# Optimization experiments

Hardware: AMD Instinct MI355X
Metric: run time of the kernel (lower is better)

The kernel has to match this reference:

```python
import jax, jax.numpy as jnp
import numpy as np
import math

B, N, D_IN, D_V, H, D_FF = 8, 2048, 256, 256, 8, 512
HD = D_V // H  # head dim = 32
EPS = 1e-5


def layernorm(x, g, b):
    mu = jnp.mean(x, axis=-1, keepdims=True)
    var = jnp.mean(jnp.square(x - mu), axis=-1, keepdims=True)
    return (x - mu) * jax.lax.rsqrt(var + EPS) * g + b


def setup_inputs() -> dict:
    key = jax.random.key(0)
    ks = jax.random.split(key, 12)
    s = 1.0 / math.sqrt(D_IN)
    return {
        "x": jax.random.normal(ks[0], (B, N, D_IN), jnp.float32),
        "y": jax.random.normal(ks[1], (B, N, D_IN), jnp.float32),
        "Wq": jax.random.normal(ks[2], (D_IN, D_V), jnp.float32) * s,
        "bq": jnp.zeros((D_V,), jnp.float32),
        "Wk": jax.random.normal(ks[3], (D_IN, D_V), jnp.float32) * s,
        "bk": jnp.zeros((D_V,), jnp.float32),
        "Wv": jax.random.normal(ks[4], (D_IN, D_V), jnp.float32) * s,
        "bv": jnp.zeros((D_V,), jnp.float32),
        "W1": jax.random.normal(ks[5], (D_V, D_FF), jnp.float32) * s,
        "b1": jnp.zeros((D_FF,), jnp.float32),
        "W2": jax.random.normal(ks[6], (D_FF, D_V), jnp.float32) * (1.0 / math.sqrt(D_FF)),
        "b2": jnp.zeros((D_V,), jnp.float32),
        "ln0_g": jnp.ones((D_IN,), jnp.float32),
        "ln0_b": jnp.zeros((D_IN,), jnp.float32),
        "ln1_g": jnp.ones((D_V,), jnp.float32),
        "ln1_b": jnp.zeros((D_V,), jnp.float32),
    }


def reference(x, y, Wq, bq, Wk, bk, Wv, bv, W1, b1, W2, b2, ln0_g, ln0_b, ln1_g, ln1_b):
    xn = layernorm(x, ln0_g, ln0_b)                      # ln0 on queries
    Q = (xn @ Wq + bq).reshape(B, N, H, HD)              # [B,Nq,H,hd]
    K = (y @ Wk + bk).reshape(B, N, H, HD)
    V = (y @ Wv + bv).reshape(B, N, H, HD)
    # NOTE: faithful scale = 1/sqrt(dim_V) (full model dim), not head dim
    S = jnp.einsum("bqhd,bkhd->bhqk", Q, K) / math.sqrt(D_V)
    A = jax.nn.softmax(S, axis=-1)
    O = Q + jnp.einsum("bhqk,bkhd->bqhd", A, V)          # per-head residual Q_ + A
    O = O.reshape(B, N, D_V)
    On = layernorm(O, ln1_g, ln1_b)
    ff = jax.nn.gelu(On @ W1 + b1, approximate=False) @ W2 + b2
    return O + ff
```

## Files before the change

kernel.cpp:

```cpp
#include <hip/hip_runtime.h>
#include <math.h>

#define RTOT 16384
#define NSEQ 2048
#define NHEAD 8
#define HDIM 32
#define QSCALE 0.09017132252479462f
#define QINV (1.0f / QSCALE)

typedef __attribute__((ext_vector_type(8))) short short8;
typedef __attribute__((ext_vector_type(4))) float f32x4;
typedef __attribute__((ext_vector_type(4))) unsigned uint4v;

#define GLOBAL_AS(p) ((__attribute__((address_space(1))) void*)(p))
#define LDS_AS(p) ((__attribute__((address_space(3))) void*)(p))

__device__ __forceinline__ unsigned pack_bf16(float a, float b) {
  unsigned ua = __float_as_uint(a) + 0x8000u;
  unsigned ub = __float_as_uint(b) + 0x8000u;
  return (ua >> 16) | (ub & 0xffff0000u);
}
__device__ __forceinline__ unsigned pack_bf16_perm(float a, float b) {
  return __builtin_amdgcn_perm(__float_as_uint(b), __float_as_uint(a),
                               0x07060302u);
}
__device__ __forceinline__ ushort bf16_1(float a) {
  return (ushort)((__float_as_uint(a) + 0x8000u) >> 16);
}
__device__ __forceinline__ float bf16_to_f(ushort u) {
  return __uint_as_float(((unsigned)u) << 16);
}
__device__ __forceinline__ short8 frag4(unsigned a0, unsigned a1, unsigned a2,
                                        unsigned a3) {
  uint4v t = {a0, a1, a2, a3};
  return __builtin_bit_cast(short8, t);
}

__global__ __launch_bounds__(256) void stage0_kernel(
    const float* __restrict__ x, const float* __restrict__ y,
    const float* __restrict__ Wq, const float* __restrict__ Wk,
    const float* __restrict__ Wv, const float* __restrict__ W1,
    const float* __restrict__ W2, const float* __restrict__ ln0g,
    const float* __restrict__ ln0b, ushort* __restrict__ Wqt,
    ushort* __restrict__ Wkt, ushort* __restrict__ Wvt,
    ushort* __restrict__ W1t, ushort* __restrict__ W2t,
    ushort* __restrict__ yh, ushort* __restrict__ xh) {
  const int bid = blockIdx.x;
  const int t = threadIdx.x;
  if (bid < 112) {
    const float* W;
    ushort* Wt;
    int K, N, tile;
    if (bid < 16) { W = Wq; Wt = Wqt; K = 256; N = 256; tile = bid; }
    else if (bid < 32) { W = Wk; Wt = Wkt; K = 256; N = 256; tile = bid - 16; }
    else if (bid < 48) { W = Wv; Wt = Wvt; K = 256; N = 256; tile = bid - 32; }
    else if (bid < 80) { W = W1; Wt = W1t; K = 256; N = 512; tile = bid - 48; }
    else { W = W2; Wt = W2t; K = 512; N = 256; tile = bid - 80; }
    const int tn = N >> 6;
    const int k0 = (tile / tn) << 6, n0 = (tile % tn) << 6;
    __shared__ float T[64][65];
#pragma unroll
    for (int i = 0; i < 16; ++i) {
      const int idx = t + i * 256;
      const int r = idx >> 6, c = idx & 63;
      T[r][c] = W[(size_t)(k0 + r) * N + n0 + c];
    }
    __syncthreads();
#pragma unroll
    for (int i = 0; i < 16; ++i) {
      const int idx = t + i * 256;
      const int r = idx >> 6, c = idx & 63;
      Wt[(size_t)(n0 + r) * K + k0 + c] = bf16_1(T[c][r]);
    }
  } else if (bid < 4208) {
    const size_t i = ((size_t)(bid - 112) * 256 + t) * 4;
    const float4 v = *(const float4*)&y[i];
    uint2 pk;
    pk.x = pack_bf16(v.x, v.y);
    pk.y = pack_bf16(v.z, v.w);
    *(uint2*)&yh[i] = pk;
  } else {
    const int lane = t & 63, wave = t >> 6;
    const size_t row = (size_t)(bid - 4208) * 4 + wave;
    const float* xr = x + row * 256;
    float4 v = *(const float4*)&xr[lane * 4];
    float s = v.x + v.y + v.z + v.w;
#pragma unroll
    for (int m = 1; m < 64; m <<= 1) s += __shfl_xor(s, m, 64);
    const float mu = s * (1.0f / 256.0f);
    const float dx = v.x - mu, dy = v.y - mu, dz = v.z - mu, dw = v.w - mu;
    float ss = dx * dx + dy * dy + dz * dz + dw * dw;
#pragma unroll
    for (int m = 1; m < 64; m <<= 1) ss += __shfl_xor(ss, m, 64);
    const float rstd = rsqrtf(ss * (1.0f / 256.0f) + 1e-5f);
    const float4 gv = *(const float4*)&ln0g[lane * 4];
    const float4 bv = *(const float4*)&ln0b[lane * 4];
    uint2 pk;
    pk.x = pack_bf16(dx * rstd * gv.x + bv.x, dy * rstd * gv.y + bv.y);
    pk.y = pack_bf16(dz * rstd * gv.z + bv.z, dw * rstd * gv.w + bv.w);
    *(uint2*)&xh[row * 256 + lane * 4] = pk;
  }
}

__global__ __launch_bounds__(256) void ln_kernel(
    const float* __restrict__ X, const float* __restrict__ g,
    const float* __restrict__ bt, ushort* __restrict__ Yh) {
  const int lane = threadIdx.x & 63;
  const int wave = threadIdx.x >> 6;
  const size_t row = (size_t)blockIdx.x * 4 + wave;
  const float* xr = X + row * 256;
  float4 v = *(const float4*)&xr[lane * 4];
  float s = v.x + v.y + v.z + v.w;
#pragma unroll
  for (int m = 1; m < 64; m <<= 1) s += __shfl_xor(s, m, 64);
  const float mu = s * (1.0f / 256.0f);
  const float dx = v.x - mu, dy = v.y - mu, dz = v.z - mu, dw = v.w - mu;
  float ss = dx * dx + dy * dy + dz * dz + dw * dw;
#pragma unroll
  for (int m = 1; m < 64; m <<= 1) ss += __shfl_xor(ss, m, 64);
  const float rstd = rsqrtf(ss * (1.0f / 256.0f) + 1e-5f);
  const float4 gv = *(const float4*)&g[lane * 4];
  const float4 bv = *(const float4*)&bt[lane * 4];
  uint2 pk;
  pk.x = pack_bf16(dx * rstd * gv.x + bv.x, dy * rstd * gv.y + bv.y);
  pk.y = pack_bf16(dz * rstd * gv.z + bv.z, dw * rstd * gv.w + bv.w);
  *(uint2*)&Yh[row * 256 + lane * 4] = pk;
}

__global__ __launch_bounds__(256) void qkv_kernel(
    const ushort* __restrict__ xh, const ushort* __restrict__ yh,
    const ushort* __restrict__ Wqt, const ushort* __restrict__ Wkt,
    const ushort* __restrict__ Wvt, const float* __restrict__ bq,
    const float* __restrict__ bk, const float* __restrict__ bv,
    ushort* __restrict__ Qh, ushort* __restrict__ Kh,
    ushort* __restrict__ VhT) {
  __shared__ union UU {
    struct { ushort As[128 * 32]; ushort Bs[64 * 32]; } s;
    ushort Ct[64 * 136];
  } u;
  const int t = threadIdx.x;
  const int lane = t & 63, wave = t >> 6;
  const int l16 = lane & 15, quad = lane >> 4;
  const int row0 = blockIdx.x * 128;
  const int ny = blockIdx.y;
  const int which = ny >> 2;
  const int n0 = (ny & 3) << 6;
  const ushort* A = (which == 2) ? xh : yh;
  const ushort* W = (which == 0) ? Wkt : (which == 1) ? Wvt : Wqt;
  const float* bs = (which == 0) ? bk : (which == 1) ? bv : bq;
  const int mrow = (wave & 1) * 64, ncol = (wave >> 1) * 32;

  const ushort* gA0 = A + (size_t)(row0 + (t >> 2)) * 256 + ((t & 3) << 3);
  const ushort* gA1 = gA0 + (size_t)64 * 256;
  const ushort* gB = W + (size_t)(n0 + (t >> 2)) * 256 + ((t & 3) << 3);
  ushort* lA0 = u.s.As + 8 * t;
  ushort* lA1 = u.s.As + 2048 + 8 * t;
  ushort* lB = u.s.Bs + 8 * t;

  f32x4 acc[4][2] = {};
  for (int kc = 0; kc < 256; kc += 32) {
    __builtin_amdgcn_global_load_lds(GLOBAL_AS(gA0 + kc), LDS_AS(lA0), 16, 0, 0);
    __builtin_amdgcn_global_load_lds(GLOBAL_AS(gA1 + kc), LDS_AS(lA1), 16, 0, 0);
    __builtin_amdgcn_global_load_lds(GLOBAL_AS(gB + kc), LDS_AS(lB), 16, 0, 0);
    __syncthreads();
    short8 af[4], bfr[2];
#pragma unroll
    for (int mi = 0; mi < 4; ++mi)
      af[mi] = *(const short8*)&u.s.As[(mrow + mi * 16 + l16) * 32 + quad * 8];
#pragma unroll
    for (int nj = 0; nj < 2; ++nj)
      bfr[nj] = *(const short8*)&u.s.Bs[(ncol + nj * 16 + l16) * 32 + quad * 8];
#pragma unroll
    for (int mi = 0; mi < 4; ++mi)
#pragma unroll
      for (int nj = 0; nj < 2; ++nj)
        acc[mi][nj] = __builtin_amdgcn_mfma_f32_16x16x32_bf16(
            af[mi], bfr[nj], acc[mi][nj], 0, 0, 0);
    __syncthreads();
  }

  if (which == 1) {
#pragma unroll
    for (int nj = 0; nj < 2; ++nj) {
      const int nloc = ncol + nj * 16 + l16;
      const float bvv = bs[n0 + nloc];
#pragma unroll
      for (int mi = 0; mi < 4; ++mi)
#pragma unroll
        for (int r = 0; r < 4; ++r)
          u.Ct[nloc * 136 + mrow + mi * 16 + quad * 4 + r] =
              bf16_1(acc[mi][nj][r] + bvv);
    }
    __syncthreads();
    const int bb = row0 >> 11, ns0 = row0 & 2047;
#pragma unroll
    for (int i = 0; i < 4; ++i) {
      const int c = t + i * 256;
      const int rr = c >> 4, c8 = (c & 15) << 3;
      *(float4*)&VhT[(size_t)(bb * 256 + n0 + rr) * 2048 + ns0 + c8] =
          *(const float4*)&u.Ct[rr * 136 + c8];
    }
  } else {
#pragma unroll
    for (int nj = 0; nj < 2; ++nj) {
      const int n = n0 + ncol + nj * 16 + l16;
      const float bvv = bs[n];
#pragma unroll
      for (int mi = 0; mi < 4; ++mi) {
#pragma unroll
        for (int r = 0; r < 4; ++r) {
          const size_t m = (size_t)row0 + mrow + mi * 16 + quad * 4 + r;
          const float v = acc[mi][nj][r] + bvv;
          if (which == 2) Qh[m * 256 + n] = bf16_1(v * QSCALE);
          else Kh[m * 256 + n] = bf16_1(v);
        }
      }
    }
  }
}

template <int MODE>
__global__ __launch_bounds__(256) void mgemm_kernel(
    const ushort* __restrict__ A, const ushort* __restrict__ Wt,
    const float* __restrict__ bias, const float* __restrict__ res,
    float* __restrict__ Cf, ushort* __restrict__ Ch, int K, int N) {
  __shared__ ushort As[128 * 32];
  __shared__ ushort Bs[64 * 32];
  const int t = threadIdx.x;
  const int lane = t & 63, wave = t >> 6;
  const int l16 = lane & 15, quad = lane >> 4;
  const int row0 = blockIdx.x * 128;
  const int n0 = blockIdx.y << 6;
  const int mrow = (wave & 1) * 64, ncol = (wave >> 1) * 32;

  const ushort* gA0 = A + (size_t)(row0 + (t >> 2)) * K + ((t & 3) << 3);
  const ushort* gA1 = gA0 + (size_t)64 * K;
  const ushort* gB = Wt + (size_t)(n0 + (t >> 2)) * K + ((t & 3) << 3);
  ushort* lA0 = As + 8 * t;
  ushort* lA1 = As + 2048 + 8 * t;
  ushort* lB = Bs + 8 * t;

  f32x4 acc[4][2] = {};
  for (int kc = 0; kc < K; kc += 32) {
    __builtin_amdgcn_global_load_lds(GLOBAL_AS(gA0 + kc), LDS_AS(lA0), 16, 0, 0);
    __builtin_amdgcn_global_load_lds(GLOBAL_AS(gA1 + kc), LDS_AS(lA1), 16, 0, 0);
    __builtin_amdgcn_global_load_lds(GLOBAL_AS(gB + kc), LDS_AS(lB), 16, 0, 0);
    __syncthreads();
    short8 af[4], bfr[2];
#pragma unroll
    for (int mi = 0; mi < 4; ++mi)
      af[mi] = *(const short8*)&As[(mrow + mi * 16 + l16) * 32 + quad * 8];
#pragma unroll
    for (int nj = 0; nj < 2; ++nj)
      bfr[nj] = *(const short8*)&Bs[(ncol + nj * 16 + l16) * 32 + quad * 8];
#pragma unroll
    for (int mi = 0; mi < 4; ++mi)
#pragma unroll
      for (int nj = 0; nj < 2; ++nj)
        acc[mi][nj] = __builtin_amdgcn_mfma_f32_16x16x32_bf16(
            af[mi], bfr[nj], acc[mi][nj], 0, 0, 0);
    __syncthreads();
  }
#pragma unroll
  for (int nj = 0; nj < 2; ++nj) {
    const int n = n0 + ncol + nj * 16 + l16;
    const float bvv = bias[n];
#pragma unroll
    for (int mi = 0; mi < 4; ++mi) {
#pragma unroll
      for (int r = 0; r < 4; ++r) {
        const size_t m = (size_t)row0 + mrow + mi * 16 + quad * 4 + r;
        float v = acc[mi][nj][r] + bvv;
        if (MODE == 2) {
          v = 0.5f * v * (1.0f + erff(v * 0.70710678118654752f));
          Ch[m * N + n] = bf16_1(v);
        }
        if (MODE == 3) Cf[m * N + n] = v + res[m * N + n];
      }
    }
  }
}

__global__ __launch_bounds__(256) void attn_kernel(
    const ushort* __restrict__ Qh, const ushort* __restrict__ Kh,
    const ushort* __restrict__ VhT, float* __restrict__ O) {
  __shared__ ushort Ks[2][128][40];
  __shared__ ushort Vt[2][32][136];

  const int t = threadIdx.x;
  const int lane = t & 63, wave = t >> 6;
  const int l16 = lane & 15, quad = lane >> 4;
  const int bh = blockIdx.x & 63;
  const int qt = blockIdx.x >> 6;
  const int b = bh >> 3, h = bh & 7;

  const size_t rowQ0 = (size_t)(b * NSEQ + qt * 128 + wave * 32 + l16);
  const short8 qfrag0 = *(const short8*)&Qh[rowQ0 * 256 + h * HDIM + quad * 8];
  const short8 qfrag1 =
      *(const short8*)&Qh[(rowQ0 + 16) * 256 + h * HDIM + quad * 8];
  const short8 ones = {16256, 16256, 16256, 16256,
                       16256, 16256, 16256, 16256};
  const f32x4 zf = {0.f, 0.f, 0.f, 0.f};

  f32x4 o00 = zf, o01 = zf, o10 = zf, o11 = zf;
  f32x4 s0 = zf, s1 = zf;

  const int kr = t >> 2, kc8 = (t & 3) << 3;
  const int krL = (kr & ~12) | ((kr & 4) << 1) | ((kr & 8) >> 1);
  const int vd = t >> 3, vc8 = (t & 7) << 3;
  const ushort* gK = Kh + ((size_t)(b * NSEQ + krL)) * 256 + h * HDIM + kc8;
  const ushort* gK2 = gK + (size_t)64 * 256;
  const ushort* gV = VhT + ((size_t)(bh * 32 + vd)) * 2048 + vc8;

  float4 kreg0 = *(const float4*)gK;
  float4 kreg1 = *(const float4*)gK2;
  float4 vreg0 = *(const float4*)gV;
  float4 vreg1 = *(const float4*)(gV + 64);

  for (int kt = 0; kt < 16; ++kt) {
    const int bf = kt & 1;
    *(float4*)&Ks[bf][kr][kc8] = kreg0;
    *(float4*)&Ks[bf][64 + kr][kc8] = kreg1;
    *(float4*)&Vt[bf][vd][vc8] = vreg0;
    *(float4*)&Vt[bf][vd][64 + vc8] = vreg1;
    __syncthreads();
    if (kt < 15) {
      const size_t ko = (size_t)(kt + 1) * 128 * 256;
      kreg0 = *(const float4*)(gK + ko);
      kreg1 = *(const float4*)(gK2 + ko);
      vreg0 = *(const float4*)(gV + (kt + 1) * 128);
      vreg1 = *(const float4*)(gV + (kt + 1) * 128 + 64);
    }

#pragma unroll
    for (int half = 0; half < 2; ++half) {
      const int r0 = half * 64;
      const int c0 = half * 64;

      short8 kf[4];
#pragma unroll
      for (int sub = 0; sub < 4; ++sub)
        kf[sub] = *(const short8*)&Ks[bf][r0 + sub * 16 + l16][quad * 8];
      const short8 vf00 = *(const short8*)&Vt[bf][l16][c0 + quad * 8];
      const short8 vf01 = *(const short8*)&Vt[bf][l16][c0 + 32 + quad * 8];
      const short8 vf10 = *(const short8*)&Vt[bf][16 + l16][c0 + quad * 8];
      const short8 vf11 = *(const short8*)&Vt[bf][16 + l16][c0 + 32 + quad * 8];

      f32x4 sa0[4], sa1[4];
#pragma unroll
      for (int sub = 0; sub < 4; ++sub)
        sa0[sub] = __builtin_amdgcn_mfma_f32_16x16x32_bf16(kf[sub], qfrag0, zf,
                                                           0, 0, 0);
#pragma unroll
      for (int sub = 0; sub < 4; ++sub)
        sa1[sub] = __builtin_amdgcn_mfma_f32_16x16x32_bf16(kf[sub], qfrag1, zf,
                                                           0, 0, 0);

      unsigned p0[4][2], p1[4][2];
#pragma unroll
      for (int sub = 0; sub < 4; ++sub) {
        p0[sub][0] = pack_bf16_perm(__builtin_amdgcn_exp2f(sa0[sub][0]),
                                    __builtin_amdgcn_exp2f(sa0[sub][1]));
        p0[sub][1] = pack_bf16_perm(__builtin_amdgcn_exp2f(sa0[sub][2]),
                                    __builtin_amdgcn_exp2f(sa0[sub][3]));
      }
#pragma unroll
      for (int sub = 0; sub < 4; ++sub) {
        p1[sub][0] = pack_bf16_perm(__builtin_amdgcn_exp2f(sa1[sub][0]),
                                    __builtin_amdgcn_exp2f(sa1[sub][1]));
        p1[sub][1] = pack_bf16_perm(__builtin_amdgcn_exp2f(sa1[sub][2]),
                                    __builtin_amdgcn_exp2f(sa1[sub][3]));
      }
      unsigned u00 = p0[0][0], w00 = p0[1][0];
      asm("v_permlane32_swap_b32 %0, %1" : "+v"(u00), "+v"(w00));
      unsigned u01 = p0[0][1], w01 = p0[1][1];
      asm("v_permlane32_swap_b32 %0, %1" : "+v"(u01), "+v"(w01));
      unsigned u02 = p0[2][0], w02 = p0[3][0];
      asm("v_permlane32_swap_b32 %0, %1" : "+v"(u02), "+v"(w02));
      unsigned u03 = p0[2][1], w03 = p0[3][1];
      asm("v_permlane32_swap_b32 %0, %1" : "+v"(u03), "+v"(w03));
      const short8 pf00 = frag4(u00, u01, w00, w01);
      const short8 pf01 = frag4(u02, u03, w02, w03);

      unsigned u10 = p1[0][0], w10 = p1[1][0];
      asm("v_permlane32_swap_b32 %0, %1" : "+v"(u10), "+v"(w10));
      unsigned u11 = p1[0][1], w11 = p1[1][1];
      asm("v_permlane32_swap_b32 %0, %1" : "+v"(u11), "+v"(w11));
      unsigned u12 = p1[2][0], w12 = p1[3][0];
      asm("v_permlane32_swap_b32 %0, %1" : "+v"(u12), "+v"(w12));
      unsigned u13 = p1[2][1], w13 = p1[3][1];
      asm("v_permlane32_swap_b32 %0, %1" : "+v"(u13), "+v"(w13));
      const short8 pf10 = frag4(u10, u11, w10, w11);
      const short8 pf11 = frag4(u12, u13, w12, w13);

      __builtin_amdgcn_s_setprio(1);
      o00 = __builtin_amdgcn_mfma_f32_16x16x32_bf16(pf00, vf00, o00, 0, 0, 0);
      o00 = __builtin_amdgcn_mfma_f32_16x16x32_bf16(pf01, vf01, o00, 0, 0, 0);
      o01 = __builtin_amdgcn_mfma_f32_16x16x32_bf16(pf00, vf10, o01, 0, 0, 0);
      o01 = __builtin_amdgcn_mfma_f32_16x16x32_bf16(pf01, vf11, o01, 0, 0, 0);
      o10 = __builtin_amdgcn_mfma_f32_16x16x32_bf16(pf10, vf00, o10, 0, 0, 0);
      o10 = __builtin_amdgcn_mfma_f32_16x16x32_bf16(pf11, vf01, o10, 0, 0, 0);
      o11 = __builtin_amdgcn_mfma_f32_16x16x32_bf16(pf10, vf10, o11, 0, 0, 0);
      o11 = __builtin_amdgcn_mfma_f32_16x16x32_bf16(pf11, vf11, o11, 0, 0, 0);
      s0 = __builtin_amdgcn_mfma_f32_16x16x32_bf16(pf00, ones, s0, 0, 0, 0);
      s0 = __builtin_amdgcn_mfma_f32_16x16x32_bf16(pf01, ones, s0, 0, 0, 0);
      s1 = __builtin_amdgcn_mfma_f32_16x16x32_bf16(pf10, ones, s1, 0, 0, 0);
      s1 = __builtin_amdgcn_mfma_f32_16x16x32_bf16(pf11, ones, s1, 0, 0, 0);
      __builtin_amdgcn_s_setprio(0);
    }
  }

#pragma unroll
  for (int g = 0; g < 2; ++g) {
    const f32x4 oS = g ? s1 : s0;
    const f32x4 oa = g ? o10 : o00;
    const f32x4 ob = g ? o11 : o01;
    const size_t row0 =
        (size_t)(b * NSEQ + qt * 128 + wave * 32 + g * 16 + quad * 4);
#pragma unroll
    for (int r = 0; r < 4; ++r) {
      const float il = 1.0f / oS[r];
      const size_t ro = (row0 + r) * 256 + h * HDIM + l16;
      O[ro] = bf16_to_f(Qh[ro]) * QINV + oa[r] * il;
      O[ro + 16] = bf16_to_f(Qh[ro + 16]) * QINV + ob[r] * il;
    }
  }
}

extern "C" void kernel_launch(void* const* d_in, const int* in_sizes, int n_in,
                              void* d_out, int out_size, void* d_ws, size_t ws_size,
                              hipStream_t stream) {
  const float* x = (const float*)d_in[0];
  const float* y = (const float*)d_in[1];
  const float* Wq = (const float*)d_in[2];
  const float* bq = (const float*)d_in[3];
  const float* Wk = (const float*)d_in[4];
  const float* bk = (const float*)d_in[5];
  const float* Wv = (const float*)d_in[6];
  const float* bv = (const float*)d_in[7];
  const float* W1 = (const float*)d_in[8];
  const float* b1 = (const float*)d_in[9];
  const float* W2 = (const float*)d_in[10];
  const float* b2 = (const float*)d_in[11];
  const float* ln0g = (const float*)d_in[12];
  const float* ln0b = (const float*)d_in[13];
  const float* ln1g = (const float*)d_in[14];
  const float* ln1b = (const float*)d_in[15];
  float* out = (float*)d_out;
  char* base = (char*)d_ws;

  const size_t RM = (size_t)RTOT * 256;
  ushort* yh = (ushort*)base;
  float* Ob = (float*)base;
  ushort* Qh = (ushort*)(base + 2 * RM * 4);
  ushort* Kh = (ushort*)(base + 2 * RM * 4 + RM * 2);
  ushort* VhT = (ushort*)(base + 3 * RM * 4);
  ushort* xh = (ushort*)(base + 3 * RM * 4 + RM * 2);
  ushort* Onh = xh;
  ushort* Hidh = Qh;
  char* wbase = base + 4 * RM * 4;
  ushort* Wqt = (ushort*)wbase;
  ushort* Wkt = Wqt + 65536;
  ushort* Wvt = Wkt + 65536;
  ushort* W1t = Wvt + 65536;
  ushort* W2t = W1t + 131072;

  stage0_kernel<<<8304, 256, 0, stream>>>(x, y, Wq, Wk, Wv, W1, W2, ln0g, ln0b,
                                          Wqt, Wkt, Wvt, W1t, W2t, yh, xh);
  qkv_kernel<<<dim3(128, 12), 256, 0, stream>>>(xh, yh, Wqt, Wkt, Wvt, bq, bk,
                                                bv, Qh, Kh, VhT);
  attn_kernel<<<1024, 256, 0, stream>>>(Qh, Kh, VhT, Ob);
  ln_kernel<<<RTOT / 4, 256, 0, stream>>>(Ob, ln1g, ln1b, Onh);
  mgemm_kernel<2><<<dim3(128, 8), 256, 0, stream>>>(Onh, W1t, b1, nullptr,
                                                    nullptr, Hidh, 256, 512);
  mgemm_kernel<3><<<dim3(128, 4), 256, 0, stream>>>(Hidh, W2t, b2, Ob, out,
                                                    nullptr, 512, 256);
}
```

Before: 216.1 us.

## Fuse K and V projections per block and use 64-row tiles for W2 GEMM

The QKV kernel now computes K and V together in one block, sharing the loaded y tile, so the grid shrinks from 12 to 8 column groups and y is read once for both projections. The Q blocks still do a single projection. The second FFN GEMM moves to a new 64x64-tile kernel with twice as many blocks, to raise occupancy and parallelism for the K=512 residual GEMM. In exchange the K/V blocks hold more accumulator registers, and the Q and K/V blocks now carry unequal amounts of work.

```diff
diff --git a/kernel.cpp b/kernel.cpp
--- a/kernel.cpp
+++ b/kernel.cpp
@@ -135,7 +135,7 @@
     ushort* __restrict__ Qh, ushort* __restrict__ Kh,
     ushort* __restrict__ VhT) {
   __shared__ union UU {
-    struct { ushort As[128 * 32]; ushort Bs[64 * 32]; } s;
+    struct { ushort As[128 * 32]; ushort Bs[2][64 * 32]; } s;
     ushort Ct[64 * 136];
   } u;
   const int t = threadIdx.x;
@@ -143,53 +143,98 @@
   const int l16 = lane & 15, quad = lane >> 4;
   const int row0 = blockIdx.x * 128;
   const int ny = blockIdx.y;
-  const int which = ny >> 2;
+  const bool isQ = ny >= 4;
   const int n0 = (ny & 3) << 6;
-  const ushort* A = (which == 2) ? xh : yh;
-  const ushort* W = (which == 0) ? Wkt : (which == 1) ? Wvt : Wqt;
-  const float* bs = (which == 0) ? bk : (which == 1) ? bv : bq;
+  const ushort* A = isQ ? xh : yh;
   const int mrow = (wave & 1) * 64, ncol = (wave >> 1) * 32;
 
   const ushort* gA0 = A + (size_t)(row0 + (t >> 2)) * 256 + ((t & 3) << 3);
   const ushort* gA1 = gA0 + (size_t)64 * 256;
-  const ushort* gB = W + (size_t)(n0 + (t >> 2)) * 256 + ((t & 3) << 3);
+  const ushort* gB0 = (isQ ? Wqt : Wkt) +
+                      (size_t)(n0 + (t >> 2)) * 256 + ((t & 3) << 3);
+  const ushort* gB1 = Wvt + (size_t)(n0 + (t >> 2)) * 256 + ((t & 3) << 3);
   ushort* lA0 = u.s.As + 8 * t;
   ushort* lA1 = u.s.As + 2048 + 8 * t;
-  ushort* lB = u.s.Bs + 8 * t;
-
-  f32x4 acc[4][2] = {};
+  ushort* lB0 = u.s.Bs[0] + 8 * t;
+  ushort* lB1 = u.s.Bs[1] + 8 * t;
+
+  f32x4 acc0[4][2] = {};
+  f32x4 acc1[4][2] = {};
   for (int kc = 0; kc < 256; kc += 32) {
     __builtin_amdgcn_global_load_lds(GLOBAL_AS(gA0 + kc), LDS_AS(lA0), 16, 0, 0);
     __builtin_amdgcn_global_load_lds(GLOBAL_AS(gA1 + kc), LDS_AS(lA1), 16, 0, 0);
-    __builtin_amdgcn_global_load_lds(GLOBAL_AS(gB + kc), LDS_AS(lB), 16, 0, 0);
-    __syncthreads();
-    short8 af[4], bfr[2];
+    __builtin_amdgcn_global_load_lds(GLOBAL_AS(gB0 + kc), LDS_AS(lB0), 16, 0, 0);
+    if (!isQ)
+      __builtin_amdgcn_global_load_lds(GLOBAL_AS(gB1 + kc), LDS_AS(lB1), 16, 0,
+                                       0);
+    __syncthreads();
+    short8 af[4], bfr0[2];
 #pragma unroll
     for (int mi = 0; mi < 4; ++mi)
       af[mi] = *(const short8*)&u.s.As[(mrow + mi * 16 + l16) * 32 + quad * 8];
 #pragma unroll
     for (int nj = 0; nj < 2; ++nj)
-      bfr[nj] = *(const short8*)&u.s.Bs[(ncol + nj * 16 + l16) * 32 + quad * 8];
+      bfr0[nj] =
+          *(const short8*)&u.s.Bs[0][(ncol + nj * 16 + l16) * 32 + quad * 8];
 #pragma unroll
     for (int mi = 0; mi < 4; ++mi)
 #pragma unroll
       for (int nj = 0; nj < 2; ++nj)
-        acc[mi][nj] = __builtin_amdgcn_mfma_f32_16x16x32_bf16(
-            af[mi], bfr[nj], acc[mi][nj], 0, 0, 0);
-    __syncthreads();
-  }
-
-  if (which == 1) {
+        acc0[mi][nj] = __builtin_amdgcn_mfma_f32_16x16x32_bf16(
+            af[mi], bfr0[nj], acc0[mi][nj], 0, 0, 0);
+    if (!isQ) {
+      short8 bfr1[2];
+#pragma unroll
+      for (int nj = 0; nj < 2; ++nj)
+        bfr1[nj] =
+            *(const short8*)&u.s.Bs[1][(ncol + nj * 16 + l16) * 32 + quad * 8];
+#pragma unroll
+      for (int mi = 0; mi < 4; ++mi)
+#pragma unroll
+        for (int nj = 0; nj < 2; ++nj)
+          acc1[mi][nj] = __builtin_amdgcn_mfma_f32_16x16x32_bf16(
+              af[mi], bfr1[nj], acc1[mi][nj], 0, 0, 0);
+    }
+    __syncthreads();
+  }
+
+  if (isQ) {
+#pragma unroll
+    for (int nj = 0; nj < 2; ++nj) {
+      const int n = n0 + ncol + nj * 16 + l16;
+      const float bvv = bq[n];
+#pragma unroll
+      for (int mi = 0; mi < 4; ++mi)
+#pragma unroll
+        for (int r = 0; r < 4; ++r) {
+          const size_t m = (size_t)row0 + mrow + mi * 16 + quad * 4 + r;
+          Qh[m * 256 + n] = bf16_1((acc0[mi][nj][r] + bvv) * QSCALE);
+        }
+    }
+  } else {
+#pragma unroll
+    for (int nj = 0; nj < 2; ++nj) {
+      const int n = n0 + ncol + nj * 16 + l16;
+      const float bvv = bk[n];
+#pragma unroll
+      for (int mi = 0; mi < 4; ++mi)
+#pragma unroll
+        for (int r = 0; r < 4; ++r) {
+          const size_t m = (size_t)row0 + mrow + mi * 16 + quad * 4 + r;
+          Kh[m * 256 + n] = bf16_1(acc0[mi][nj][r] + bvv);
+        }
+    }
+    __syncthreads();
 #pragma unroll
     for (int nj = 0; nj < 2; ++nj) {
       const int nloc = ncol + nj * 16 + l16;
-      const float bvv = bs[n0 + nloc];
+      const float bvv = bv[n0 + nloc];
 #pragma unroll
       for (int mi = 0; mi < 4; ++mi)
 #pragma unroll
         for (int r = 0; r < 4; ++r)
           u.Ct[nloc * 136 + mrow + mi * 16 + quad * 4 + r] =
-              bf16_1(acc[mi][nj][r] + bvv);
+              bf16_1(acc1[mi][nj][r] + bvv);
     }
     __syncthreads();
     const int bb = row0 >> 11, ns0 = row0 & 2047;
@@ -200,30 +245,12 @@
       *(float4*)&VhT[(size_t)(bb * 256 + n0 + rr) * 2048 + ns0 + c8] =
           *(const float4*)&u.Ct[rr * 136 + c8];
     }
-  } else {
-#pragma unroll
-    for (int nj = 0; nj < 2; ++nj) {
-      const int n = n0 + ncol + nj * 16 + l16;
-      const float bvv = bs[n];
-#pragma unroll
-      for (int mi = 0; mi < 4; ++mi) {
-#pragma unroll
-        for (int r = 0; r < 4; ++r) {
-          const size_t m = (size_t)row0 + mrow + mi * 16 + quad * 4 + r;
-          const float v = acc[mi][nj][r] + bvv;
-          if (which == 2) Qh[m * 256 + n] = bf16_1(v * QSCALE);
-          else Kh[m * 256 + n] = bf16_1(v);
-        }
-      }
-    }
-  }
-}
-
-template <int MODE>
+  }
+}
+
 __global__ __launch_bounds__(256) void mgemm_kernel(
     const ushort* __restrict__ A, const ushort* __restrict__ Wt,
-    const float* __restrict__ bias, const float* __restrict__ res,
-    float* __restrict__ Cf, ushort* __restrict__ Ch, int K, int N) {
+    const float* __restrict__ bias, ushort* __restrict__ Ch, int K, int N) {
   __shared__ ushort As[128 * 32];
   __shared__ ushort Bs[64 * 32];
   const int t = threadIdx.x;
@@ -271,11 +298,61 @@
       for (int r = 0; r < 4; ++r) {
         const size_t m = (size_t)row0 + mrow + mi * 16 + quad * 4 + r;
         float v = acc[mi][nj][r] + bvv;
-        if (MODE == 2) {
-          v = 0.5f * v * (1.0f + erff(v * 0.70710678118654752f));
-          Ch[m * N + n] = bf16_1(v);
-        }
-        if (MODE == 3) Cf[m * N + n] = v + res[m * N + n];
+        v = 0.5f * v * (1.0f + erff(v * 0.70710678118654752f));
+        Ch[m * N + n] = bf16_1(v);
+      }
+    }
+  }
+}
+
+__global__ __launch_bounds__(256) void mgemm64_kernel(
+    const ushort* __restrict__ A, const ushort* __restrict__ Wt,
+    const float* __restrict__ bias, const float* __restrict__ res,
+    float* __restrict__ Cf, int K, int N) {
+  __shared__ ushort As[64 * 32];
+  __shared__ ushort Bs[64 * 32];
+  const int t = threadIdx.x;
+  const int lane = t & 63, wave = t >> 6;
+  const int l16 = lane & 15, quad = lane >> 4;
+  const int row0 = blockIdx.x * 64;
+  const int n0 = blockIdx.y << 6;
+  const int mrow = (wave & 1) * 32, ncol = (wave >> 1) * 32;
+
+  const ushort* gA = A + (size_t)(row0 + (t >> 2)) * K + ((t & 3) << 3);
+  const ushort* gB = Wt + (size_t)(n0 + (t >> 2)) * K + ((t & 3) << 3);
+  ushort* lA = As + 8 * t;
+  ushort* lB = Bs + 8 * t;
+
+  f32x4 acc[2][2] = {};
+  for (int kc = 0; kc < K; kc += 32) {
+    __builtin_amdgcn_global_load_lds(GLOBAL_AS(gA + kc), LDS_AS(lA), 16, 0, 0);
+    __builtin_amdgcn_global_load_lds(GLOBAL_AS(gB + kc), LDS_AS(lB), 16, 0, 0);
+    __syncthreads();
+    short8 af[2], bfr[2];
+#pragma unroll
+    for (int mi = 0; mi < 2; ++mi)
+      af[mi] = *(const short8*)&As[(mrow + mi * 16 + l16) * 32 + quad * 8];
+#pragma unroll
+    for (int nj = 0; nj < 2; ++nj)
+      bfr[nj] = *(const short8*)&Bs[(ncol + nj * 16 + l16) * 32 + quad * 8];
+#pragma unroll
+    for (int mi = 0; mi < 2; ++mi)
+#pragma unroll
+      for (int nj = 0; nj < 2; ++nj)
+        acc[mi][nj] = __builtin_amdgcn_mfma_f32_16x16x32_bf16(
+            af[mi], bfr[nj], acc[mi][nj], 0, 0, 0);
+    __syncthreads();
+  }
+#pragma unroll
+  for (int nj = 0; nj < 2; ++nj) {
+    const int n = n0 + ncol + nj * 16 + l16;
+    const float bvv = bias[n];
+#pragma unroll
+    for (int mi = 0; mi < 2; ++mi) {
+#pragma unroll
+      for (int r = 0; r < 4; ++r) {
+        const size_t m = (size_t)row0 + mrow + mi * 16 + quad * 4 + r;
+        Cf[m * N + n] = acc[mi][nj][r] + bvv + res[m * N + n];
       }
     }
   }
@@ -467,12 +544,11 @@
 
   stage0_kernel<<<8304, 256, 0, stream>>>(x, y, Wq, Wk, Wv, W1, W2, ln0g, ln0b,
                                           Wqt, Wkt, Wvt, W1t, W2t, yh, xh);
-  qkv_kernel<<<dim3(128, 12), 256, 0, stream>>>(xh, yh, Wqt, Wkt, Wvt, bq, bk,
-                                                bv, Qh, Kh, VhT);
+  qkv_kernel<<<dim3(128, 8), 256, 0, stream>>>(xh, yh, Wqt, Wkt, Wvt, bq, bk,
+                                               bv, Qh, Kh, VhT);
   attn_kernel<<<1024, 256, 0, stream>>>(Qh, Kh, VhT, Ob);
   ln_kernel<<<RTOT / 4, 256, 0, stream>>>(Ob, ln1g, ln1b, Onh);
-  mgemm_kernel<2><<<dim3(128, 8), 256, 0, stream>>>(Onh, W1t, b1, nullptr,
-                                                    nullptr, Hidh, 256, 512);
-  mgemm_kernel<3><<<dim3(128, 4), 256, 0, stream>>>(Hidh, W2t, b2, Ob, out,
-                                                    nullptr, 512, 256);
-}
+  mgemm_kernel<<<dim3(128, 8), 256, 0, stream>>>(Onh, W1t, b1, Hidh, 256, 512);
+  mgemm64_kernel<<<dim3(256, 4), 256, 0, stream>>>(Hidh, W2t, b2, Ob, out, 512,
+                                                   256);
+}
```

Measured after the change: 212.6 us. About the same (-1.6%).
